# Kernel optimization log

Measured on AMD Instinct MI355X. Metric: run time of the kernel, lower is better.

## Reference

```python
import jax, jax.numpy as jnp
import numpy as np

STRIDE = 1
PAD = 1
EXTENT = 3  # kernel footprint (ceil of max tap offset), 3x3 tap grid


def setup_inputs() -> dict:
    key = jax.random.key(0)
    k1, k2 = jax.random.split(key)
    B, Cin, H, W = 8, 64, 128, 128
    Cout, K = 64, 9
    x = jax.random.normal(k1, (B, Cin, H, W), dtype=jnp.float32)
    # per-tap weights, one scalar weight per (out_ch, in_ch, tap) -- op formula is 'x * w'
    weights = jax.random.normal(k2, (Cout, Cin, K), dtype=jnp.float32) * 0.05
    # 3x3 integer grid shifted by +0.4 -> non-integer offsets => bilinear (sub-pixel) gather
    base = jnp.stack(jnp.meshgrid(jnp.arange(3.0), jnp.arange(3.0), indexing='ij'), -1).reshape(9, 2)
    tap_offsets = (base + 0.4).astype(jnp.float32)  # [K, 2] (dy, dx)
    return {"x": x, "weights": weights, "tap_offsets": tap_offsets}


def _bilinear_tap(xp, dy, dx, H_out, W_out):
    # Gather xp at (oy*stride + dy, ox*stride + dx) with separable bilinear interp.
    Hp, Wp = xp.shape[-2], xp.shape[-1]
    y = jnp.arange(H_out, dtype=xp.dtype) * STRIDE + dy
    xc = jnp.arange(W_out, dtype=xp.dtype) * STRIDE + dx
    y0 = jnp.floor(y)
    x0 = jnp.floor(xc)
    fy = (y - y0)[None, None, :, None]
    fx = (xc - x0)[None, None, None, :]
    y0i = jnp.clip(y0.astype(jnp.int32), 0, Hp - 1)
    y1i = jnp.clip(y0.astype(jnp.int32) + 1, 0, Hp - 1)
    x0i = jnp.clip(x0.astype(jnp.int32), 0, Wp - 1)
    x1i = jnp.clip(x0.astype(jnp.int32) + 1, 0, Wp - 1)
    # interp rows first: [B, C, H_out, Wp]
    ry = xp[:, :, y0i, :] * (1.0 - fy) + xp[:, :, y1i, :] * fy
    # then columns: [B, C, H_out, W_out]
    return ry[:, :, :, x0i] * (1.0 - fx) + ry[:, :, :, x1i] * fx


def reference(x, weights, tap_offsets):
    B, Cin, H, W = x.shape
    K = weights.shape[-1]
    xp = jnp.pad(x, ((0, 0), (0, 0), (PAD, PAD), (PAD, PAD)))
    H_out = (H + 2 * PAD - EXTENT) // STRIDE + 1
    W_out = (W + 2 * PAD - EXTENT) // STRIDE + 1
    # gather all taps (loop over small fixed K=9, each fully vectorized over B,C,H,W)
    taps = [_bilinear_tap(xp, tap_offsets[k, 0], tap_offsets[k, 1], H_out, W_out)
            for k in range(K)]
    g = jnp.stack(taps, 0)  # [K, B, Cin, H_out, W_out]
    # per-tap op 'x * w', accumulated over taps and input channels
    return jnp.einsum('kbiyx,oik->boyx', g, weights)  # [B, Cout, H_out, W_out]
```

## Files before the change

### kernel.cpp

```cpp
#include <hip/hip_runtime.h>


#define CIN   64
#define COUT  64
#define HH    128
#define WW    128

typedef __attribute__((ext_vector_type(8))) short bf16x8;
typedef __attribute__((ext_vector_type(4))) float f32x4;
typedef __attribute__((ext_vector_type(4))) unsigned int u32x4;

__device__ __forceinline__ unsigned short f2bf(float f) {
  unsigned int u = __float_as_uint(f);
  u = (u + 0x7fffu + ((u >> 16) & 1u)) >> 16;
  return (unsigned short)u;
}

__device__ __forceinline__ unsigned int cvtpk(float lo, float hi) {
  unsigned int r;
  asm("v_cvt_pk_bf16_f32 %0, %1, %2" : "=v"(r) : "v"(lo), "v"(hi));
  return r;
}

__global__ void make_wb(const float* __restrict__ wgt,
                        const float* __restrict__ off,
                        unsigned short* __restrict__ wb2)
{
  int id = blockIdx.x * 64 + threadIdx.x;
  int o = id >> 6, c = id & 63;
  float W16[16];
  #pragma unroll
  for (int i = 0; i < 16; ++i) W16[i] = 0.f;
  for (int k = 0; k < 9; ++k) {
    float dy = off[2*k], dx = off[2*k+1];
    float fyf = floorf(dy), fxf = floorf(dx);
    int   iy = (int)fyf,   ix = (int)fxf;
    float fy = dy - fyf,   fx = dx - fxf;
    float wk = wgt[(o*CIN + c)*9 + k];
    W16[(iy  )*4 + ix  ] += wk * (1.f-fy)*(1.f-fx);
    W16[(iy  )*4 + ix+1] += wk * (1.f-fy)*fx;
    W16[(iy+1)*4 + ix  ] += wk * fy*(1.f-fx);
    W16[(iy+1)*4 + ix+1] += wk * fy*fx;
  }
  int p = c >> 5, q = (c >> 3) & 3, j = c & 7;
  int n = o >> 4, m15 = o & 15;
  int lanei = q*16 + m15;
  for (int rs = 0; rs < 16; ++rs)
    wb2[(size_t)(((p*16 + rs)*4 + n)*64 + lanei)*8 + j] = f2bf(W16[rs]);
}

__global__ __launch_bounds__(64, 2)
void conv_mfma(const float* __restrict__ x,
               const unsigned short* __restrict__ wb2,
               float* __restrict__ out)
{
  __shared__ __align__(16) char lds[17408];

  const int wg  = blockIdx.x;
  const int xcd = wg & 7;
  const int i   = wg >> 3;
  const int b   = i >> 5;
  const int r5  = i & 31;
  const int y0  = xcd * 16 + (r5 >> 1);
  const int x0  = (r5 & 1) * 64;
  const int lane = threadIdx.x;
  const int m15  = lane & 15;
  const int q    = lane >> 4;

  int gx   = x0 - 1 + lane;
  bool gxv = ((unsigned)gx < (unsigned)WW);
  int gxc  = gx < 0 ? 0 : (gx > WW-1 ? WW-1 : gx);
  const int he = (lane >> 4) < 3 ? (lane >> 4) : 2;
  int gxh  = x0 + 63 + he;
  bool gxhv = ((unsigned)gxh < (unsigned)WW) && (lane < 48);
  int gxhc = gxh > WW-1 ? WW-1 : gxh;
  const int hp = lane & 15;
  const int hoff = (64 + he)*64 + ((hp >> 2) & 3)*16 + (hp & 3)*4;

  int stoff[4];
  #pragma unroll
  for (int c = 0; c < 4; ++c)
    stoff[c] = lane*64 + ((c + (lane >> 2)) & 3)*16;

  int aoff[4];
  #pragma unroll
  for (int s = 0; s < 4; ++s) {
    int c0 = m15 + s;
    aoff[s] = c0*64 + ((q + (c0 >> 2)) & 3)*16;
  }

  f32x4 acc[4][4];
  #pragma unroll
  for (int mi = 0; mi < 4; ++mi)
    #pragma unroll
    for (int nn = 0; nn < 4; ++nn)
      acc[mi][nn] = (f32x4){0.f, 0.f, 0.f, 0.f};

  float GM0[32], GM1[32], GH0[2], GH1[2];

  auto LOADP = [&](int k, float* GM, float* GH) {
    int gy = y0 + (k & 3) - 1;
    if ((unsigned)gy < (unsigned)HH) {
      const float* ps = x + ((size_t)((b*CIN + (k >> 2)*32)*HH + gy))*WW;
      #pragma unroll
      for (int cc = 0; cc < 32; ++cc) GM[cc] = ps[(size_t)cc*HH*WW + gxc];
      GH[0] = ps[(size_t)(2*hp    )*HH*WW + gxhc];
      GH[1] = ps[(size_t)(2*hp + 1)*HH*WW + gxhc];
    }
  };

  auto WRITEP = [&](int k, const float* GM, const float* GH) {
    int gy = y0 + (k & 3) - 1;
    char* base = lds + (k & 1)*4352;
    if ((unsigned)gy < (unsigned)HH) {
      #pragma unroll
      for (int c = 0; c < 4; ++c) {
        unsigned int pk[4];
        #pragma unroll
        for (int w = 0; w < 4; ++w) {
          pk[w] = cvtpk(GM[c*8 + 2*w], GM[c*8 + 2*w + 1]);
          pk[w] = gxv ? pk[w] : 0u;
        }
        *(u32x4*)(base + stoff[c]) = *(u32x4*)pk;
      }
      unsigned int hw = cvtpk(GH[0], GH[1]);
      hw = gxhv ? hw : 0u;
      if (lane < 48) *(unsigned int*)(base + hoff) = hw;
    } else {
      #pragma unroll
      for (int c = 0; c < 4; ++c)
        *(u32x4*)(base + stoff[c]) = (u32x4){0u,0u,0u,0u};
      if (lane < 48) *(unsigned int*)(base + hoff) = 0u;
    }
  };

  auto COMPUTE = [&](int k) {
    const char* wpB = (const char*)wb2 + (size_t)(k >> 2)*65536 + (size_t)lane*16;
    const char* ab  = lds + (k & 1)*4352;
    const int r4 = (k & 3)*4;
    #pragma unroll
    for (int s = 0; s < 4; ++s) {
      const char* wrow = wpB + (size_t)(r4 + s)*4096;
      bf16x8 bfr[4], afr[4];
      #pragma unroll
      for (int n = 0; n < 4; ++n)
        bfr[n] = *(const bf16x8*)(wrow + n*1024);
      #pragma unroll
      for (int mi = 0; mi < 4; ++mi)
        afr[mi] = *(const bf16x8*)(ab + aoff[s] + mi*1024);
      #pragma unroll
      for (int mi = 0; mi < 4; ++mi)
        #pragma unroll
        for (int nn = 0; nn < 4; ++nn)
          acc[mi][nn] = __builtin_amdgcn_mfma_f32_16x16x32_bf16(afr[mi], bfr[nn], acc[mi][nn], 0, 0, 0);
    }
  };

  LOADP(0, GM0, GH0);
  LOADP(1, GM1, GH1);
  WRITEP(0, GM0, GH0);
  #pragma unroll
  for (int kk = 0; kk < 4; ++kk) {
    if (kk < 3) LOADP(2*kk + 2, GM0, GH0);
    WRITEP(2*kk + 1, GM1, GH1);
    COMPUTE(2*kk);
    if (kk < 3) {
      LOADP(2*kk + 3, GM1, GH1);
      WRITEP(2*kk + 2, GM0, GH0);
    }
    COMPUTE(2*kk + 1);
  }

  float* epi = (float*)lds;
  #pragma unroll
  for (int mi = 0; mi < 4; ++mi)
    #pragma unroll
    for (int nn = 0; nn < 4; ++nn) {
      int o  = nn*16 + m15;
      int px = mi*16 + q*4;
      *(f32x4*)&epi[o*68 + px] = acc[mi][nn];
    }
  #pragma unroll
  for (int i2 = 0; i2 < 16; ++i2) {
    int o  = i2*4 + q;
    int px = m15*4;
    f32x4 v = *(const f32x4*)&epi[o*68 + px];
    *(f32x4*)&out[(((size_t)(b*COUT + o))*HH + y0)*WW + x0 + px] = v;
  }
}

extern "C" void kernel_launch(void* const* d_in, const int* in_sizes, int n_in,
                              void* d_out, int out_size, void* d_ws, size_t ws_size,
                              hipStream_t stream)
{
  const float* x   = (const float*)d_in[0];
  const float* wgt = (const float*)d_in[1];
  const float* off = (const float*)d_in[2];
  float* out = (float*)d_out;
  unsigned short* wb2 = (unsigned short*)d_ws;

  make_wb<<<64, 64, 0, stream>>>(wgt, off, wb2);
  conv_mfma<<<2048, 64, 0, stream>>>(x, wb2, out);
}
```

Measured before the change: 106.7 us.

## Compute two output rows per workgroup to reuse shared input rows

Each workgroup now produces two adjacent output rows instead of one. It streams five input rows per channel half rather than four, and feeds each staged row into two accumulator sets with the matching shifted weight rows. This removes redundant global loads and bf16 conversion of the overlapping input rows, and the grid is halved to match. In exchange, accumulator register use doubles and the register prefetch drops from double to single buffering. Fewer workgroups also lowers the available parallelism.

```diff
diff --git a/kernel.cpp b/kernel.cpp
--- a/kernel.cpp
+++ b/kernel.cpp
@@ -59,10 +59,10 @@
   const int wg  = blockIdx.x;
   const int xcd = wg & 7;
   const int i   = wg >> 3;
-  const int b   = i >> 5;
-  const int r5  = i & 31;
-  const int y0  = xcd * 16 + (r5 >> 1);
-  const int x0  = (r5 & 1) * 64;
+  const int b   = i >> 4;
+  const int r4  = i & 15;
+  const int y0  = xcd * 16 + (r4 >> 1) * 2;
+  const int x0  = (r4 & 1) * 64;
   const int lane = threadIdx.x;
   const int m15  = lane & 15;
   const int q    = lane >> 4;
@@ -89,19 +89,21 @@
     aoff[s] = c0*64 + ((q + (c0 >> 2)) & 3)*16;
   }
 
-  f32x4 acc[4][4];
+  f32x4 acc0[4][4], acc1[4][4];
   #pragma unroll
   for (int mi = 0; mi < 4; ++mi)
     #pragma unroll
-    for (int nn = 0; nn < 4; ++nn)
-      acc[mi][nn] = (f32x4){0.f, 0.f, 0.f, 0.f};
-
-  float GM0[32], GM1[32], GH0[2], GH1[2];
-
-  auto LOADP = [&](int k, float* GM, float* GH) {
-    int gy = y0 + (k & 3) - 1;
+    for (int nn = 0; nn < 4; ++nn) {
+      acc0[mi][nn] = (f32x4){0.f, 0.f, 0.f, 0.f};
+      acc1[mi][nn] = (f32x4){0.f, 0.f, 0.f, 0.f};
+    }
+
+  float GM[32], GH[2];
+
+  auto LOADP = [&](int k) {
+    int gy = y0 + (k % 5) - 1;
     if ((unsigned)gy < (unsigned)HH) {
-      const float* ps = x + ((size_t)((b*CIN + (k >> 2)*32)*HH + gy))*WW;
+      const float* ps = x + ((size_t)((b*CIN + (k / 5)*32)*HH + gy))*WW;
       #pragma unroll
       for (int cc = 0; cc < 32; ++cc) GM[cc] = ps[(size_t)cc*HH*WW + gxc];
       GH[0] = ps[(size_t)(2*hp    )*HH*WW + gxhc];
@@ -109,8 +111,8 @@
     }
   };
 
-  auto WRITEP = [&](int k, const float* GM, const float* GH) {
-    int gy = y0 + (k & 3) - 1;
+  auto WRITEP = [&](int k) {
+    int gy = y0 + (k % 5) - 1;
     char* base = lds + (k & 1)*4352;
     if ((unsigned)gy < (unsigned)HH) {
       #pragma unroll
@@ -135,40 +137,46 @@
   };
 
   auto COMPUTE = [&](int k) {
-    const char* wpB = (const char*)wb2 + (size_t)(k >> 2)*65536 + (size_t)lane*16;
-    const char* ab  = lds + (k & 1)*4352;
-    const int r4 = (k & 3)*4;
+    const int r = k % 5;
+    const char* ab = lds + (k & 1)*4352;
+    const char* wb = (const char*)wb2 + (size_t)(k / 5)*65536 + (size_t)lane*16;
     #pragma unroll
     for (int s = 0; s < 4; ++s) {
-      const char* wrow = wpB + (size_t)(r4 + s)*4096;
-      bf16x8 bfr[4], afr[4];
-      #pragma unroll
-      for (int n = 0; n < 4; ++n)
-        bfr[n] = *(const bf16x8*)(wrow + n*1024);
+      bf16x8 afr[4];
       #pragma unroll
       for (int mi = 0; mi < 4; ++mi)
         afr[mi] = *(const bf16x8*)(ab + aoff[s] + mi*1024);
-      #pragma unroll
-      for (int mi = 0; mi < 4; ++mi)
-        #pragma unroll
-        for (int nn = 0; nn < 4; ++nn)
-          acc[mi][nn] = __builtin_amdgcn_mfma_f32_16x16x32_bf16(afr[mi], bfr[nn], acc[mi][nn], 0, 0, 0);
+      if (r < 4) {
+        const char* w0 = wb + (size_t)(r*4 + s)*4096;
+        bf16x8 b0[4];
+        #pragma unroll
+        for (int n = 0; n < 4; ++n) b0[n] = *(const bf16x8*)(w0 + n*1024);
+        #pragma unroll
+        for (int mi = 0; mi < 4; ++mi)
+          #pragma unroll
+          for (int nn = 0; nn < 4; ++nn)
+            acc0[mi][nn] = __builtin_amdgcn_mfma_f32_16x16x32_bf16(afr[mi], b0[nn], acc0[mi][nn], 0, 0, 0);
+      }
+      if (r >= 1) {
+        const char* w1 = wb + (size_t)((r-1)*4 + s)*4096;
+        bf16x8 b1[4];
+        #pragma unroll
+        for (int n = 0; n < 4; ++n) b1[n] = *(const bf16x8*)(w1 + n*1024);
+        #pragma unroll
+        for (int mi = 0; mi < 4; ++mi)
+          #pragma unroll
+          for (int nn = 0; nn < 4; ++nn)
+            acc1[mi][nn] = __builtin_amdgcn_mfma_f32_16x16x32_bf16(afr[mi], b1[nn], acc1[mi][nn], 0, 0, 0);
+      }
     }
   };
 
-  LOADP(0, GM0, GH0);
-  LOADP(1, GM1, GH1);
-  WRITEP(0, GM0, GH0);
-  #pragma unroll
-  for (int kk = 0; kk < 4; ++kk) {
-    if (kk < 3) LOADP(2*kk + 2, GM0, GH0);
-    WRITEP(2*kk + 1, GM1, GH1);
-    COMPUTE(2*kk);
-    if (kk < 3) {
-      LOADP(2*kk + 3, GM1, GH1);
-      WRITEP(2*kk + 2, GM0, GH0);
-    }
-    COMPUTE(2*kk + 1);
+  LOADP(0);
+  #pragma unroll
+  for (int k = 0; k < 10; ++k) {
+    WRITEP(k);
+    if (k < 9) LOADP(k + 1);
+    COMPUTE(k);
   }
 
   float* epi = (float*)lds;
@@ -178,7 +186,7 @@
     for (int nn = 0; nn < 4; ++nn) {
       int o  = nn*16 + m15;
       int px = mi*16 + q*4;
-      *(f32x4*)&epi[o*68 + px] = acc[mi][nn];
+      *(f32x4*)&epi[o*68 + px] = acc0[mi][nn];
     }
   #pragma unroll
   for (int i2 = 0; i2 < 16; ++i2) {
@@ -186,6 +194,21 @@
     int px = m15*4;
     f32x4 v = *(const f32x4*)&epi[o*68 + px];
     *(f32x4*)&out[(((size_t)(b*COUT + o))*HH + y0)*WW + x0 + px] = v;
+  }
+  #pragma unroll
+  for (int mi = 0; mi < 4; ++mi)
+    #pragma unroll
+    for (int nn = 0; nn < 4; ++nn) {
+      int o  = nn*16 + m15;
+      int px = mi*16 + q*4;
+      *(f32x4*)&epi[o*68 + px] = acc1[mi][nn];
+    }
+  #pragma unroll
+  for (int i2 = 0; i2 < 16; ++i2) {
+    int o  = i2*4 + q;
+    int px = m15*4;
+    f32x4 v = *(const f32x4*)&epi[o*68 + px];
+    *(f32x4*)&out[(((size_t)(b*COUT + o))*HH + (y0 + 1))*WW + x0 + px] = v;
   }
 }
 
@@ -200,5 +223,5 @@
   unsigned short* wb2 = (unsigned short*)d_ws;
 
   make_wb<<<64, 64, 0, stream>>>(wgt, off, wb2);
-  conv_mfma<<<2048, 64, 0, stream>>>(x, wb2, out);
-}
+  conv_mfma<<<1024, 64, 0, stream>>>(x, wb2, out);
+}
```

New measurement: 158.1 us. 48.2% more time.
